# Kernel optimization log

Measured on AMD Instinct MI355X. Metric: run time of the kernel, lower is better.

Reference implementation:

```python
import jax, jax.numpy as jnp
import numpy as np

C, NH, NP = 512, 8, 4
HD = C // NH
H = W = D = 20
N = H * W * D
B = 2
EPS = 1e-5


def _layer_norm(x, g, b):
    mu = jnp.mean(x, axis=-1, keepdims=True)
    var = jnp.var(x, axis=-1, keepdims=True)
    return (x - mu) * jax.lax.rsqrt(var + EPS) * g + b


def setup_inputs() -> dict:
    key = jax.random.key(0)
    ks = jax.random.split(key, 10)

    def lin(k, fan_in, shape, scale=1.0):
        return (jax.random.normal(k, shape, jnp.float32) / np.float32(np.sqrt(fan_in))) * scale

    return {
        "f_query": jax.random.normal(ks[0], (B, C, H, W, D), jnp.float32),
        "f_kv": jax.random.normal(ks[1], (B, C, H, W, D), jnp.float32),
        "ln_g": jnp.ones((C,), jnp.float32),
        "ln_b": jnp.zeros((C,), jnp.float32),
        "Wq": lin(ks[2], C, (C, C)),
        "bq": jnp.zeros((C,), jnp.float32),
        "Wo1": lin(ks[3], C, (C, C)),
        "bo1": jnp.zeros((C,), jnp.float32),
        "Wo2": lin(ks[4], C, (C, NH * NP * 3), 0.1),  # small nonzero so interpolation is exercised
        "bo2": jnp.zeros((NH * NP * 3,), jnp.float32),
        "Wa": lin(ks[5], C, (C, NH * NP)),
        "ba": jnp.zeros((NH * NP,), jnp.float32),
        "Wout": lin(ks[6], C, (C, C)),
        "bout": jnp.zeros((C,), jnp.float32),
    }


def reference(f_query, f_kv, ln_g, ln_b, Wq, bq, Wo1, bo1, Wo2, bo2, Wa, ba, Wout, bout):
    # tokens: flatten (H,W,D) in row-major order, matching torch .flatten(2)
    fq = jnp.transpose(f_query.reshape(B, C, N), (0, 2, 1))  # (B,N,C)
    q = _layer_norm(fq, ln_g, ln_b)
    Q = q @ Wq + bq  # (B,N,C)

    off = jnp.clip(jax.nn.relu(Q @ Wo1 + bo1) @ Wo2 + bo2, -3.0, 3.0)
    off = off.reshape(B, N, NH, NP, 3)
    attn = jax.nn.softmax((Q @ Wa + ba).reshape(B, N, NH, NP), axis=-1)

    gy, gx, gz = jnp.meshgrid(jnp.arange(H, dtype=jnp.float32),
                              jnp.arange(W, dtype=jnp.float32),
                              jnp.arange(D, dtype=jnp.float32), indexing='ij')
    base = jnp.stack([gy, gx, gz], -1).reshape(N, 3)  # (N,3) in (y,x,z)
    locs = base[None, :, None, None, :] + off         # (B,N,NH,NP,3)

    # normalization exactly as original module (ch0 by H, ch1 by W, ch2 by D)
    n0 = 2.0 * locs[..., 0] / (H - 1) - 1.0
    n1 = 2.0 * locs[..., 1] / (W - 1) - 1.0
    n2 = 2.0 * locs[..., 2] / (D - 1) - 1.0
    # torch grid_sample on input permuted to (B,c,D,H,W): grid ch0->x (W axis),
    # ch1->y (H axis), ch2->z (D axis); align_corners=True; border padding = clip
    ix = jnp.clip((n0 + 1.0) * 0.5 * (W - 1), 0.0, W - 1)
    iy = jnp.clip((n1 + 1.0) * 0.5 * (H - 1), 0.0, H - 1)
    iz = jnp.clip((n2 + 1.0) * 0.5 * (D - 1), 0.0, D - 1)

    x0 = jnp.floor(ix); y0 = jnp.floor(iy); z0 = jnp.floor(iz)
    fx = (ix - x0)[..., None]; fy = (iy - y0)[..., None]; fz = (iz - z0)[..., None]
    x0i = x0.astype(jnp.int32); y0i = y0.astype(jnp.int32); z0i = z0.astype(jnp.int32)
    x1i = jnp.minimum(x0i + 1, W - 1)
    y1i = jnp.minimum(y0i + 1, H - 1)
    z1i = jnp.minimum(z0i + 1, D - 1)

    # f_kv (B,C,H,W,D) -> per-head channels-last volume (B,NH,D,H,W,HD)
    feats = jnp.transpose(f_kv.reshape(B, NH, HD, H, W, D), (0, 1, 5, 3, 4, 2))
    bi = jnp.arange(B)[:, None, None, None]
    hi = jnp.arange(NH)[None, None, :, None]

    def g(zi, yi, xi):
        return feats[bi, hi, zi, yi, xi]  # (B,N,NH,NP,HD)

    sampled = (
        g(z0i, y0i, x0i) * (1 - fz) * (1 - fy) * (1 - fx)
        + g(z0i, y0i, x1i) * (1 - fz) * (1 - fy) * fx
        + g(z0i, y1i, x0i) * (1 - fz) * fy * (1 - fx)
        + g(z0i, y1i, x1i) * (1 - fz) * fy * fx
        + g(z1i, y0i, x0i) * fz * (1 - fy) * (1 - fx)
        + g(z1i, y0i, x1i) * fz * (1 - fy) * fx
        + g(z1i, y1i, x0i) * fz * fy * (1 - fx)
        + g(z1i, y1i, x1i) * fz * fy * fx
    )  # (B,N,NH,NP,HD)

    out = jnp.einsum('bnhp,bnhpc->bnhc', attn, sampled).reshape(B, N, C)
    out = out @ Wout + bout
    return jnp.transpose(out, (0, 2, 1)).reshape(B, C, H, W, D)
```

## Files before the change

### kernel.cpp

```cpp
#include <hip/hip_runtime.h>
#include <math.h>

#define C_DIM 512
#define NHEAD 8
#define HDIM 64
#define NTOK 8000
#define BN_TOK 16000

typedef __attribute__((ext_vector_type(8))) _Float16 f16x8;
typedef __attribute__((ext_vector_type(4))) float f32x4;
typedef __attribute__((ext_vector_type(2))) _Float16 h2;
typedef unsigned short u16;

__device__ __forceinline__ int imin(int a, int b) { return a < b ? a : b; }

__device__ __forceinline__ u16 f2h(float x) {
    _Float16 h = (_Float16)x;
    return __builtin_bit_cast(u16, h);
}

__device__ __forceinline__ size_t aidx(int t, int c) {
    return ((size_t)(t >> 4)) * 8192 + (size_t)((c >> 5) * 512
         + (((c >> 3) & 3) * 128) + ((t & 15) * 8) + (c & 7));
}
__device__ __forceinline__ size_t bidx(int n, int k) {
    return ((size_t)(n >> 4)) * 8192 + (size_t)((k >> 5) * 512
         + (((k >> 3) & 3) * 128) + ((n & 15) * 8) + (k & 7));
}

__device__ __forceinline__ void async16(const void* g, void* l) {
    __builtin_amdgcn_global_load_lds(
        (const __attribute__((address_space(1))) void*)g,
        (__attribute__((address_space(3))) void*)l, 16, 0, 0);
}

__device__ __forceinline__ f32x4 agload16(const u16* p) {
    f32x4 r;
    asm volatile("global_load_dwordx4 %0, %1, off" : "=v"(r) : "v"(p));
    return r;
}

#define VMWAIT(N) do { asm volatile("s_waitcnt vmcnt(" #N ")"); \
                       __builtin_amdgcn_sched_barrier(0); } while (0)

__global__ __launch_bounds__(256) void transpose_c2l_f16(
    const float* __restrict__ in, u16* __restrict__ out)
{
    __shared__ float tile[32][33];
    int b = blockIdx.z;
    const float* inb = in + (size_t)b * 512 * NTOK;
    u16* outb = out + (size_t)b * NTOK * 512;
    int s0 = blockIdx.x * 32, r0 = blockIdx.y * 32;
    int tx = threadIdx.x & 31, ty = threadIdx.x >> 5;
#pragma unroll
    for (int i = 0; i < 4; i++)
        tile[ty + i * 8][tx] = inb[(size_t)(r0 + ty + i * 8) * NTOK + s0 + tx];
    __syncthreads();
    int rq = threadIdx.x & 7, sy = threadIdx.x >> 3;
    ushort4 o;
    o.x = f2h(tile[rq * 4 + 0][sy]);
    o.y = f2h(tile[rq * 4 + 1][sy]);
    o.z = f2h(tile[rq * 4 + 2][sy]);
    o.w = f2h(tile[rq * 4 + 3][sy]);
    *reinterpret_cast<ushort4*>(outb + (size_t)(s0 + sy) * 512 + r0 + rq * 4) = o;
}

__global__ __launch_bounds__(256) void wcvt_all(
    const float* __restrict__ W0, u16* __restrict__ T0,
    const float* __restrict__ W1, u16* __restrict__ T1,
    const float* __restrict__ W2, u16* __restrict__ T2,
    const float* __restrict__ W3, u16* __restrict__ T3,
    const float* __restrict__ W4, u16* __restrict__ T4)
{
    const float* W; u16* Wt; int Nout, Npad;
    switch (blockIdx.z) {
        case 0: W = W0; Wt = T0; Nout = 512; Npad = 512; break;
        case 1: W = W1; Wt = T1; Nout = 512; Npad = 512; break;
        case 2: W = W2; Wt = T2; Nout = 512; Npad = 512; break;
        case 3: W = W3; Wt = T3; Nout = 96;  Npad = 128; break;
        default: W = W4; Wt = T4; Nout = 32; Npad = 128; break;
    }
    int blocked = (blockIdx.z != 2);
    int n0 = blockIdx.x * 32, k0 = blockIdx.y * 32;
    if (n0 >= Npad) return;
    __shared__ float t[32][33];
    int tx = threadIdx.x & 31, ty = threadIdx.x >> 5;
#pragma unroll
    for (int i = 0; i < 4; i++) {
        int k = k0 + ty + i * 8, n = n0 + tx;
        t[ty + i * 8][tx] = (n < Nout) ? W[(size_t)k * Nout + n] : 0.f;
    }
    __syncthreads();
#pragma unroll
    for (int i = 0; i < 4; i++) {
        int n = n0 + ty + i * 8, k = k0 + tx;
        u16 v = f2h(t[tx][ty + i * 8]);
        if (blocked) Wt[bidx(n, k)] = v;
        else         Wt[(size_t)n * 512 + k] = v;
    }
}

__device__ __forceinline__ void lds_gemm64(
    const u16* Tin, u16* Tout, const u16* __restrict__ Wblk,
    const float* __restrict__ bias, int relu, int lane, int wv)
{
    int ml = lane & 15, quad = lane >> 4;
    int c0 = wv * 64;
    const u16* Bp = Wblk + (size_t)(c0 >> 4) * 8192 + (size_t)lane * 8;

    f32x4 acc[4][4];
#pragma unroll
    for (int t = 0; t < 4; t++)
#pragma unroll
        for (int j = 0; j < 4; j++) acc[t][j] = (f32x4){0.f, 0.f, 0.f, 0.f};

    f32x4 bfr[4][4];
#pragma unroll
    for (int kb = 0; kb < 3; kb++)
#pragma unroll
        for (int j = 0; j < 4; j++)
            bfr[kb][j] = agload16(Bp + (size_t)j * 8192 + kb * 512);

#pragma unroll
    for (int kk = 0; kk < 16; kk++) {
        if (kk + 3 < 16) {
#pragma unroll
            for (int j = 0; j < 4; j++)
                bfr[(kk + 3) & 3][j] = agload16(
                    Bp + (size_t)j * 8192 + (kk + 3) * 512);
        }
        f16x8 a[4];
#pragma unroll
        for (int t = 0; t < 4; t++)
            a[t] = *reinterpret_cast<const f16x8*>(
                Tin + (t * 16 + ml) * 520 + (kk * 4 + quad) * 8);
        if (kk < 13)       VMWAIT(12);
        else if (kk == 13) VMWAIT(8);
        else if (kk == 14) VMWAIT(4);
        else               VMWAIT(0);
#pragma unroll
        for (int j = 0; j < 4; j++) {
            f16x8 bj = __builtin_bit_cast(f16x8, bfr[kk & 3][j]);
#pragma unroll
            for (int t = 0; t < 4; t++)
                acc[t][j] = __builtin_amdgcn_mfma_f32_16x16x32_f16(
                    a[t], bj, acc[t][j], 0, 0, 0);
        }
    }

#pragma unroll
    for (int t = 0; t < 4; t++)
#pragma unroll
        for (int j = 0; j < 4; j++) {
            int col = c0 + j * 16 + ml;
            float bia = bias[col];
#pragma unroll
            for (int rg = 0; rg < 4; rg++) {
                float v = acc[t][j][rg] + bia;
                if (relu) v = fmaxf(v, 0.f);
                Tout[(t * 16 + quad * 4 + rg) * 520 + col] = f2h(v);
            }
        }
}

__global__ __launch_bounds__(512, 2) void mlp_fused(
    const float* __restrict__ fq, const float* __restrict__ gamma,
    const float* __restrict__ beta,
    const u16* __restrict__ Wqb, const float* __restrict__ bq,
    const u16* __restrict__ Wo1b, const float* __restrict__ bo1,
    const u16* __restrict__ Wo2b, const float* __restrict__ bo2,
    const u16* __restrict__ Wab, const float* __restrict__ ba,
    float* __restrict__ offb, float* __restrict__ lgb)
{
    __shared__ u16 T0[64 * 520], T1[64 * 520];
    __shared__ float ps[64][9], pq[64][9];
    __shared__ float muA[64], rsA[64];
    int tid = threadIdx.x, lane = tid & 63, wv = tid >> 6;
    int blk = blockIdx.x;
    int tp = tid & 63;
    int cg = tid >> 6;
    int b = blk >= 125;
    int n0 = (blk - b * 125) * 64;
    const float* src = fq + (size_t)b * C_DIM * NTOK + n0 + tp;

    float vals[64];
    {
        float s = 0.f, q = 0.f;
#pragma unroll
        for (int it = 0; it < 8; ++it) {
            int c0 = (cg + it * 8) * 8;
#pragma unroll
            for (int e = 0; e < 8; ++e) {
                float v = src[(size_t)(c0 + e) * NTOK];
                vals[it * 8 + e] = v;
                s += v; q += v * v;
            }
        }
        ps[tp][cg] = s; pq[tp][cg] = q;
    }
    __syncthreads();
    if (tid < 64) {
        float S = 0.f, SQ = 0.f;
#pragma unroll
        for (int g = 0; g < 8; ++g) { S += ps[tid][g]; SQ += pq[tid][g]; }
        float mu = S * (1.f / 512.f);
        muA[tid] = mu;
        rsA[tid] = rsqrtf(SQ * (1.f / 512.f) - mu * mu + 1e-5f);
    }
    __syncthreads();
    {
        float mu = muA[tp], rs = rsA[tp];
#pragma unroll
        for (int it = 0; it < 8; ++it) {
            int c0 = (cg + it * 8) * 8;
            u16 o[8];
#pragma unroll
            for (int e = 0; e < 8; ++e)
                o[e] = f2h((vals[it * 8 + e] - mu) * rs * gamma[c0 + e]
                           + beta[c0 + e]);
            *reinterpret_cast<f16x8*>(&T0[tp * 520 + c0]) =
                *reinterpret_cast<const f16x8*>(o);
        }
    }
    __syncthreads();
    lds_gemm64(T0, T1, Wqb, bq, 0, lane, wv);
    __syncthreads();
    lds_gemm64(T1, T0, Wo1b, bo1, 1, lane, wv);
    __syncthreads();
    {
        int ml = lane & 15, quad = lane >> 4;
        int isLg = wv >= 6;
        int cb = isLg ? (wv - 6) : wv;
        const u16* Tin = isLg ? T1 : T0;
        const u16* Wsm = isLg ? Wab : Wo2b;
        const float* bs = isLg ? ba : bo2;
        float* outg = isLg ? lgb : offb;
        int ldo = isLg ? 32 : 96;
        const u16* Wp = Wsm + (size_t)cb * 8192 + (size_t)lane * 8;
        f16x8 wb[16];
#pragma unroll
        for (int kk = 0; kk < 16; kk++)
            wb[kk] = *reinterpret_cast<const f16x8*>(Wp + (size_t)kk * 512);
        float bia = bs[cb * 16 + ml];
        int tbase = blk * 64;
#pragma unroll
        for (int tg = 0; tg < 4; tg++) {
            f32x4 acc = (f32x4){0.f, 0.f, 0.f, 0.f};
            const u16* Ar = Tin + (tg * 16 + ml) * 520;
#pragma unroll
            for (int kk = 0; kk < 16; kk++) {
                f16x8 af = *reinterpret_cast<const f16x8*>(
                    Ar + (kk * 4 + quad) * 8);
                acc = __builtin_amdgcn_mfma_f32_16x16x32_f16(
                    af, wb[kk], acc, 0, 0, 0);
            }
#pragma unroll
            for (int rg = 0; rg < 4; rg++)
                outg[(size_t)(tbase + tg * 16 + quad * 4 + rg) * ldo
                     + cb * 16 + ml] = acc[rg] + bia;
        }
    }
}

__device__ __forceinline__ void ws_body512(
    const u16* __restrict__ A, const u16* __restrict__ Bp,
    const float* __restrict__ bias, float* __restrict__ Cf,
    int colBase, int mt)
{
    __shared__ u16 Bs[64 * 512];
    int tid = threadIdx.x, lane = tid & 63, wv = tid >> 6;

#pragma unroll
    for (int c = 0; c < 8; c++) {
        int id = c * 512 + tid;
        int row = id >> 6, seg = id & 63;
        async16(Bp + (size_t)row * 512 + ((seg ^ (row & 7)) << 3),
                Bs + (size_t)id * 8);
    }

    int ml = lane & 15, quad = lane >> 4;
    int wm = (wv >> 1) * 64, wn = (wv & 1) * 32;

    int rowj[2];
#pragma unroll
    for (int j = 0; j < 2; j++) rowj[j] = wn + j * 16 + ml;

    __syncthreads();

    int bm = mt * 256;
    const u16* Ap = A + ((size_t)((bm + wm) >> 4)) * 8192 + (size_t)lane * 8;

    f32x4 acc[4][2];
#pragma unroll
    for (int i = 0; i < 4; i++)
#pragma unroll
        for (int j = 0; j < 2; j++) acc[i][j] = (f32x4){0.f, 0.f, 0.f, 0.f};

    f32x4 afr[4][4];
    f16x8 bf[2][2];

#pragma unroll
    for (int kb = 0; kb < 3; kb++)
#pragma unroll
        for (int i = 0; i < 4; i++)
            afr[kb][i] = agload16(Ap + (size_t)i * 8192 + kb * 512);
#pragma unroll
    for (int j = 0; j < 2; j++)
        bf[0][j] = *reinterpret_cast<const f16x8*>(
            Bs + (size_t)rowj[j] * 512 + (((0 + quad) ^ (rowj[j] & 7)) << 3));

#pragma unroll
    for (int kk = 0; kk < 16; kk++) {
        if (kk + 3 < 16) {
#pragma unroll
            for (int i = 0; i < 4; i++)
                afr[(kk + 3) & 3][i] = agload16(
                    Ap + (size_t)i * 8192 + (kk + 3) * 512);
        }
        if (kk + 1 < 16) {
#pragma unroll
            for (int j = 0; j < 2; j++) {
                int seg = (kk + 1) * 4 + quad;
                bf[(kk + 1) & 1][j] = *reinterpret_cast<const f16x8*>(
                    Bs + (size_t)rowj[j] * 512 + ((seg ^ (rowj[j] & 7)) << 3));
            }
        }
        if (kk < 13)       VMWAIT(12);
        else if (kk == 13) VMWAIT(8);
        else if (kk == 14) VMWAIT(4);
        else               VMWAIT(0);
#pragma unroll
        for (int i = 0; i < 4; i++)
#pragma unroll
            for (int j = 0; j < 2; j++)
                acc[i][j] = __builtin_amdgcn_mfma_f32_16x16x32_f16(
                    __builtin_bit_cast(f16x8, afr[kk & 3][i]),
                    bf[kk & 1][j], acc[i][j], 0, 0, 0);
    }

#pragma unroll
    for (int i = 0; i < 4; i++) {
        int row = bm + wm + i * 16 + quad * 4;
        if (row >= BN_TOK) continue;
#pragma unroll
        for (int j = 0; j < 2; j++) {
            int col = colBase + wn + j * 16 + ml;
            float bia = bias[col];
            int bb = row >= 8000;
            float4 st;
            st.x = acc[i][j][0] + bia;
            st.y = acc[i][j][1] + bia;
            st.z = acc[i][j][2] + bia;
            st.w = acc[i][j][3] + bia;
            *reinterpret_cast<float4*>(
                Cf + ((size_t)(bb * 512 + col)) * 8000 + (row - bb * 8000)) = st;
        }
    }
}

__global__ __launch_bounds__(512, 4) void gemm_out(
    const u16* __restrict__ A, const u16* __restrict__ WT,
    const float* __restrict__ bias, float* __restrict__ Cf)
{
    int did = blockIdx.x;
    int m = ((did >> 6) << 3) | (did & 7);
    if (m >= 63) return;
    int p = (did >> 3) & 7;
    ws_body512(A, WT + (size_t)p * 64 * 512, bias, Cf, p * 64, m);
}

__global__ __launch_bounds__(256) void sample_kernel(
    const u16* __restrict__ vol, const float* __restrict__ offb,
    const float* __restrict__ lgb, u16* __restrict__ outp)
{
    int wid = threadIdx.x >> 6, lane = threadIdx.x & 63;
    int bx = blockIdx.x;
    int bn = ((bx & 7) * 500 + (bx >> 3)) * 4 + wid;
    int h = lane >> 3, cl = lane & 7;
    int b = bn / NTOK, n = bn - b * NTOK;
    int y = n / 400;
    int r2 = n - y * 400;
    int x = r2 / 20;
    int z = r2 - x * 20;

    const float* op = offb + (size_t)bn * 96 + h * 12;
    const float* lp = lgb + (size_t)bn * 32 + h * 4;
    float l0 = lp[0], l1 = lp[1], l2 = lp[2], l3 = lp[3];
    float mx = fmaxf(fmaxf(l0, l1), fmaxf(l2, l3));
    float e0 = expf(l0 - mx), e1 = expf(l1 - mx), e2 = expf(l2 - mx), e3 = expf(l3 - mx);
    float inv = 1.f / (e0 + e1 + e2 + e3);
    float at[4] = {e0 * inv, e1 * inv, e2 * inv, e3 * inv};

    const u16* volb = vol + b * (NTOK * C_DIM) + h * HDIM + cl * 8;
    h2 acc0 = (h2)(_Float16)0, acc1 = acc0, acc2 = acc0, acc3 = acc0;
#pragma unroll 1
    for (int p = 0; p < 4; p++) {
        float o0 = fminf(fmaxf(op[p * 3 + 0], -3.f), 3.f);
        float o1 = fminf(fmaxf(op[p * 3 + 1], -3.f), 3.f);
        float o2 = fminf(fmaxf(op[p * 3 + 2], -3.f), 3.f);
        float ix = fminf(fmaxf((float)y + o0, 0.f), 19.f);
        float iy = fminf(fmaxf((float)x + o1, 0.f), 19.f);
        float iz = fminf(fmaxf((float)z + o2, 0.f), 19.f);
        float xf = floorf(ix), yf = floorf(iy), zf = floorf(iz);
        float fx = ix - xf, fy = iy - yf, fz = iz - zf;
        int x0 = (int)xf, y0 = (int)yf, z0 = (int)zf;
        int x1 = imin(x0 + 1, 19), y1 = imin(y0 + 1, 19), z1 = imin(z0 + 1, 19);
        int s00 = y0 * 400 + x0 * 20, s01 = y0 * 400 + x1 * 20;
        int s10 = y1 * 400 + x0 * 20, s11 = y1 * 400 + x1 * 20;
        uint4 v000 = *(const uint4*)(volb + (s00 + z0) * C_DIM);
        uint4 v001 = *(const uint4*)(volb + (s01 + z0) * C_DIM);
        uint4 v010 = *(const uint4*)(volb + (s10 + z0) * C_DIM);
        uint4 v011 = *(const uint4*)(volb + (s11 + z0) * C_DIM);
        uint4 v100 = *(const uint4*)(volb + (s00 + z1) * C_DIM);
        uint4 v101 = *(const uint4*)(volb + (s01 + z1) * C_DIM);
        uint4 v110 = *(const uint4*)(volb + (s10 + z1) * C_DIM);
        uint4 v111 = *(const uint4*)(volb + (s11 + z1) * C_DIM);
        float wz0 = (1.f - fz) * at[p], wz1 = fz * at[p];
        float w00 = wz0 * (1.f - fy), w01 = wz0 * fy;
        float w10 = wz1 * (1.f - fy), w11 = wz1 * fy;
        float gx0 = 1.f - fx;
        float cw[8] = { w00 * gx0, w00 * fx, w01 * gx0, w01 * fx,
                        w10 * gx0, w10 * fx, w11 * gx0, w11 * fx };
        const uint4* cv[8] = { &v000, &v001, &v010, &v011,
                               &v100, &v101, &v110, &v111 };
#pragma unroll
        for (int c = 0; c < 8; c++) {
            _Float16 wh = (_Float16)cw[c];
            h2 w2; w2.x = wh; w2.y = wh;
            uint4 d = *cv[c];
            acc0 += __builtin_bit_cast(h2, d.x) * w2;
            acc1 += __builtin_bit_cast(h2, d.y) * w2;
            acc2 += __builtin_bit_cast(h2, d.z) * w2;
            acc3 += __builtin_bit_cast(h2, d.w) * w2;
        }
    }
    uint4 o;
    o.x = __builtin_bit_cast(unsigned, acc0);
    o.y = __builtin_bit_cast(unsigned, acc1);
    o.z = __builtin_bit_cast(unsigned, acc2);
    o.w = __builtin_bit_cast(unsigned, acc3);
    *reinterpret_cast<uint4*>(outp + aidx(bn, h * HDIM + cl * 8)) = o;
}

extern "C" void kernel_launch(void* const* d_in, const int* in_sizes, int n_in,
                              void* d_out, int out_size, void* d_ws, size_t ws_size,
                              hipStream_t stream)
{
    const float* f_query = (const float*)d_in[0];
    const float* f_kv    = (const float*)d_in[1];
    const float* ln_g    = (const float*)d_in[2];
    const float* ln_b    = (const float*)d_in[3];
    const float* Wq      = (const float*)d_in[4];
    const float* bq      = (const float*)d_in[5];
    const float* Wo1     = (const float*)d_in[6];
    const float* bo1     = (const float*)d_in[7];
    const float* Wo2     = (const float*)d_in[8];
    const float* bo2     = (const float*)d_in[9];
    const float* Wa      = (const float*)d_in[10];
    const float* ba      = (const float*)d_in[11];
    const float* Wout    = (const float*)d_in[12];
    const float* bout    = (const float*)d_in[13];
    float* out = (float*)d_out;

    float* ws = (float*)d_ws;
    float* offb = ws;
    float* lgb  = ws + 1536000;
    u16* kvT   = (u16*)(ws + 2048000);
    u16* qb    = kvT  + 8192000;
    u16* WqT   = qb   + 8192000;
    u16* Wo1T  = WqT + 262144;
    u16* WoutT = Wo1T + 262144;
    u16* Wo2T  = WoutT + 262144;
    u16* WaT   = Wo2T + 65536;

    dim3 blk(256);
    dim3 blk512(512);
    wcvt_all<<<dim3(16, 16, 5), blk, 0, stream>>>(
        Wq, WqT, Wo1, Wo1T, Wout, WoutT, Wo2, Wo2T, Wa, WaT);
    transpose_c2l_f16<<<dim3(250, 16, 2), blk, 0, stream>>>(f_kv, kvT);
    mlp_fused<<<dim3(250), blk512, 0, stream>>>(
        f_query, ln_g, ln_b, WqT, bq, Wo1T, bo1, Wo2T, bo2, WaT, ba,
        offb, lgb);
    sample_kernel<<<dim3(4000), blk, 0, stream>>>(kvT, offb, lgb, qb);
    gemm_out<<<dim3(512), blk512, 0, stream>>>(qb, WoutT, bout, out);
}
```

Measured before the change: 194.8 us.

## Fuse trilinear sampling with output projection and merge prep kernels

The deformable sampling now writes each 64-token tile into LDS and immediately multiplies it by Wout with MFMA in the same block, so the separate sampled-feature buffer and the gemm_out kernel go away. The weight conversion and the f_kv transpose are merged into one launch. This removes a 16 MB intermediate write and read plus two kernel launches. In exchange only 250 blocks of 512 threads do the gather-heavy sampling, where the old sampling kernel used 4000 blocks, so latency hiding and occupancy during the gather may suffer. The Wout layout also changes from row-major to blocked.

```diff
diff --git a/kernel.cpp b/kernel.cpp
--- a/kernel.cpp
+++ b/kernel.cpp
@@ -19,19 +19,9 @@
     return __builtin_bit_cast(u16, h);
 }
 
-__device__ __forceinline__ size_t aidx(int t, int c) {
-    return ((size_t)(t >> 4)) * 8192 + (size_t)((c >> 5) * 512
-         + (((c >> 3) & 3) * 128) + ((t & 15) * 8) + (c & 7));
-}
 __device__ __forceinline__ size_t bidx(int n, int k) {
     return ((size_t)(n >> 4)) * 8192 + (size_t)((k >> 5) * 512
          + (((k >> 3) & 3) * 128) + ((n & 15) * 8) + (k & 7));
-}
-
-__device__ __forceinline__ void async16(const void* g, void* l) {
-    __builtin_amdgcn_global_load_lds(
-        (const __attribute__((address_space(1))) void*)g,
-        (__attribute__((address_space(3))) void*)l, 16, 0, 0);
 }
 
 __device__ __forceinline__ f32x4 agload16(const u16* p) {
@@ -43,60 +33,60 @@
 #define VMWAIT(N) do { asm volatile("s_waitcnt vmcnt(" #N ")"); \
                        __builtin_amdgcn_sched_barrier(0); } while (0)
 
-__global__ __launch_bounds__(256) void transpose_c2l_f16(
-    const float* __restrict__ in, u16* __restrict__ out)
+__global__ __launch_bounds__(256) void prep_all(
+    const float* __restrict__ f_kv, u16* __restrict__ kvT,
+    const float* __restrict__ W0, u16* __restrict__ T0w,
+    const float* __restrict__ W1, u16* __restrict__ T1w,
+    const float* __restrict__ W2, u16* __restrict__ T2w,
+    const float* __restrict__ W3, u16* __restrict__ T3w,
+    const float* __restrict__ W4, u16* __restrict__ T4w)
 {
     __shared__ float tile[32][33];
-    int b = blockIdx.z;
-    const float* inb = in + (size_t)b * 512 * NTOK;
-    u16* outb = out + (size_t)b * NTOK * 512;
-    int s0 = blockIdx.x * 32, r0 = blockIdx.y * 32;
-    int tx = threadIdx.x & 31, ty = threadIdx.x >> 5;
-#pragma unroll
-    for (int i = 0; i < 4; i++)
-        tile[ty + i * 8][tx] = inb[(size_t)(r0 + ty + i * 8) * NTOK + s0 + tx];
-    __syncthreads();
-    int rq = threadIdx.x & 7, sy = threadIdx.x >> 3;
-    ushort4 o;
-    o.x = f2h(tile[rq * 4 + 0][sy]);
-    o.y = f2h(tile[rq * 4 + 1][sy]);
-    o.z = f2h(tile[rq * 4 + 2][sy]);
-    o.w = f2h(tile[rq * 4 + 3][sy]);
-    *reinterpret_cast<ushort4*>(outb + (size_t)(s0 + sy) * 512 + r0 + rq * 4) = o;
-}
-
-__global__ __launch_bounds__(256) void wcvt_all(
-    const float* __restrict__ W0, u16* __restrict__ T0,
-    const float* __restrict__ W1, u16* __restrict__ T1,
-    const float* __restrict__ W2, u16* __restrict__ T2,
-    const float* __restrict__ W3, u16* __restrict__ T3,
-    const float* __restrict__ W4, u16* __restrict__ T4)
-{
-    const float* W; u16* Wt; int Nout, Npad;
-    switch (blockIdx.z) {
-        case 0: W = W0; Wt = T0; Nout = 512; Npad = 512; break;
-        case 1: W = W1; Wt = T1; Nout = 512; Npad = 512; break;
-        case 2: W = W2; Wt = T2; Nout = 512; Npad = 512; break;
-        case 3: W = W3; Wt = T3; Nout = 96;  Npad = 128; break;
-        default: W = W4; Wt = T4; Nout = 32; Npad = 128; break;
-    }
-    int blocked = (blockIdx.z != 2);
-    int n0 = blockIdx.x * 32, k0 = blockIdx.y * 32;
-    if (n0 >= Npad) return;
-    __shared__ float t[32][33];
-    int tx = threadIdx.x & 31, ty = threadIdx.x >> 5;
-#pragma unroll
-    for (int i = 0; i < 4; i++) {
-        int k = k0 + ty + i * 8, n = n0 + tx;
-        t[ty + i * 8][tx] = (n < Nout) ? W[(size_t)k * Nout + n] : 0.f;
-    }
-    __syncthreads();
-#pragma unroll
-    for (int i = 0; i < 4; i++) {
-        int n = n0 + ty + i * 8, k = k0 + tx;
-        u16 v = f2h(t[tx][ty + i * 8]);
-        if (blocked) Wt[bidx(n, k)] = v;
-        else         Wt[(size_t)n * 512 + k] = v;
+    int id = blockIdx.x;
+    if (id < 8000) {
+        int b = id / 4000, r = id - b * 4000;
+        int s0 = (r % 250) * 32, r0 = (r / 250) * 32;
+        const float* inb = f_kv + (size_t)b * 512 * NTOK;
+        u16* outb = kvT + (size_t)b * NTOK * 512;
+        int tx = threadIdx.x & 31, ty = threadIdx.x >> 5;
+#pragma unroll
+        for (int i = 0; i < 4; i++)
+            tile[ty + i * 8][tx] =
+                inb[(size_t)(r0 + ty + i * 8) * NTOK + s0 + tx];
+        __syncthreads();
+        int rq = threadIdx.x & 7, sy = threadIdx.x >> 3;
+        ushort4 o;
+        o.x = f2h(tile[rq * 4 + 0][sy]);
+        o.y = f2h(tile[rq * 4 + 1][sy]);
+        o.z = f2h(tile[rq * 4 + 2][sy]);
+        o.w = f2h(tile[rq * 4 + 3][sy]);
+        *reinterpret_cast<ushort4*>(
+            outb + (size_t)(s0 + sy) * 512 + r0 + rq * 4) = o;
+    } else {
+        int id2 = id - 8000;
+        int z = id2 >> 8, xy = id2 & 255;
+        int n0 = (xy & 15) * 32, k0 = (xy >> 4) * 32;
+        const float* W; u16* Wt; int Nout, Npad;
+        switch (z) {
+            case 0: W = W0; Wt = T0w; Nout = 512; Npad = 512; break;
+            case 1: W = W1; Wt = T1w; Nout = 512; Npad = 512; break;
+            case 2: W = W2; Wt = T2w; Nout = 512; Npad = 512; break;
+            case 3: W = W3; Wt = T3w; Nout = 96;  Npad = 128; break;
+            default: W = W4; Wt = T4w; Nout = 32; Npad = 128; break;
+        }
+        if (n0 >= Npad) return;
+        int tx = threadIdx.x & 31, ty = threadIdx.x >> 5;
+#pragma unroll
+        for (int i = 0; i < 4; i++) {
+            int k = k0 + ty + i * 8, n = n0 + tx;
+            tile[ty + i * 8][tx] = (n < Nout) ? W[(size_t)k * Nout + n] : 0.f;
+        }
+        __syncthreads();
+#pragma unroll
+        for (int i = 0; i < 4; i++) {
+            int n = n0 + ty + i * 8, k = k0 + tx;
+            Wt[bidx(n, k)] = f2h(tile[tx][ty + i * 8]);
+        }
     }
 }
 
@@ -262,184 +252,155 @@
     }
 }
 
-__device__ __forceinline__ void ws_body512(
-    const u16* __restrict__ A, const u16* __restrict__ Bp,
-    const float* __restrict__ bias, float* __restrict__ Cf,
-    int colBase, int mt)
+__global__ __launch_bounds__(512, 2) void sample_out(
+    const u16* __restrict__ vol, const float* __restrict__ offb,
+    const float* __restrict__ lgb, const u16* __restrict__ Woutb,
+    const float* __restrict__ bout, float* __restrict__ outp)
 {
-    __shared__ u16 Bs[64 * 512];
+    __shared__ u16 T0[64 * 520];
     int tid = threadIdx.x, lane = tid & 63, wv = tid >> 6;
-
-#pragma unroll
-    for (int c = 0; c < 8; c++) {
-        int id = c * 512 + tid;
-        int row = id >> 6, seg = id & 63;
-        async16(Bp + (size_t)row * 512 + ((seg ^ (row & 7)) << 3),
-                Bs + (size_t)id * 8);
-    }
-
-    int ml = lane & 15, quad = lane >> 4;
-    int wm = (wv >> 1) * 64, wn = (wv & 1) * 32;
-
-    int rowj[2];
-#pragma unroll
-    for (int j = 0; j < 2; j++) rowj[j] = wn + j * 16 + ml;
-
-    __syncthreads();
-
-    int bm = mt * 256;
-    const u16* Ap = A + ((size_t)((bm + wm) >> 4)) * 8192 + (size_t)lane * 8;
-
-    f32x4 acc[4][2];
-#pragma unroll
-    for (int i = 0; i < 4; i++)
-#pragma unroll
-        for (int j = 0; j < 2; j++) acc[i][j] = (f32x4){0.f, 0.f, 0.f, 0.f};
-
-    f32x4 afr[4][4];
-    f16x8 bf[2][2];
-
-#pragma unroll
-    for (int kb = 0; kb < 3; kb++)
-#pragma unroll
-        for (int i = 0; i < 4; i++)
-            afr[kb][i] = agload16(Ap + (size_t)i * 8192 + kb * 512);
-#pragma unroll
-    for (int j = 0; j < 2; j++)
-        bf[0][j] = *reinterpret_cast<const f16x8*>(
-            Bs + (size_t)rowj[j] * 512 + (((0 + quad) ^ (rowj[j] & 7)) << 3));
-
-#pragma unroll
-    for (int kk = 0; kk < 16; kk++) {
-        if (kk + 3 < 16) {
-#pragma unroll
-            for (int i = 0; i < 4; i++)
-                afr[(kk + 3) & 3][i] = agload16(
-                    Ap + (size_t)i * 8192 + (kk + 3) * 512);
-        }
-        if (kk + 1 < 16) {
-#pragma unroll
-            for (int j = 0; j < 2; j++) {
-                int seg = (kk + 1) * 4 + quad;
-                bf[(kk + 1) & 1][j] = *reinterpret_cast<const f16x8*>(
-                    Bs + (size_t)rowj[j] * 512 + ((seg ^ (rowj[j] & 7)) << 3));
-            }
-        }
-        if (kk < 13)       VMWAIT(12);
-        else if (kk == 13) VMWAIT(8);
-        else if (kk == 14) VMWAIT(4);
-        else               VMWAIT(0);
-#pragma unroll
-        for (int i = 0; i < 4; i++)
-#pragma unroll
-            for (int j = 0; j < 2; j++)
-                acc[i][j] = __builtin_amdgcn_mfma_f32_16x16x32_f16(
-                    __builtin_bit_cast(f16x8, afr[kk & 3][i]),
-                    bf[kk & 1][j], acc[i][j], 0, 0, 0);
-    }
-
-#pragma unroll
-    for (int i = 0; i < 4; i++) {
-        int row = bm + wm + i * 16 + quad * 4;
-        if (row >= BN_TOK) continue;
-#pragma unroll
-        for (int j = 0; j < 2; j++) {
-            int col = colBase + wn + j * 16 + ml;
-            float bia = bias[col];
-            int bb = row >= 8000;
-            float4 st;
-            st.x = acc[i][j][0] + bia;
-            st.y = acc[i][j][1] + bia;
-            st.z = acc[i][j][2] + bia;
-            st.w = acc[i][j][3] + bia;
-            *reinterpret_cast<float4*>(
-                Cf + ((size_t)(bb * 512 + col)) * 8000 + (row - bb * 8000)) = st;
-        }
-    }
-}
-
-__global__ __launch_bounds__(512, 4) void gemm_out(
-    const u16* __restrict__ A, const u16* __restrict__ WT,
-    const float* __restrict__ bias, float* __restrict__ Cf)
-{
-    int did = blockIdx.x;
-    int m = ((did >> 6) << 3) | (did & 7);
-    if (m >= 63) return;
-    int p = (did >> 3) & 7;
-    ws_body512(A, WT + (size_t)p * 64 * 512, bias, Cf, p * 64, m);
-}
-
-__global__ __launch_bounds__(256) void sample_kernel(
-    const u16* __restrict__ vol, const float* __restrict__ offb,
-    const float* __restrict__ lgb, u16* __restrict__ outp)
-{
-    int wid = threadIdx.x >> 6, lane = threadIdx.x & 63;
-    int bx = blockIdx.x;
-    int bn = ((bx & 7) * 500 + (bx >> 3)) * 4 + wid;
-    int h = lane >> 3, cl = lane & 7;
-    int b = bn / NTOK, n = bn - b * NTOK;
-    int y = n / 400;
-    int r2 = n - y * 400;
-    int x = r2 / 20;
-    int z = r2 - x * 20;
-
-    const float* op = offb + (size_t)bn * 96 + h * 12;
-    const float* lp = lgb + (size_t)bn * 32 + h * 4;
-    float l0 = lp[0], l1 = lp[1], l2 = lp[2], l3 = lp[3];
-    float mx = fmaxf(fmaxf(l0, l1), fmaxf(l2, l3));
-    float e0 = expf(l0 - mx), e1 = expf(l1 - mx), e2 = expf(l2 - mx), e3 = expf(l3 - mx);
-    float inv = 1.f / (e0 + e1 + e2 + e3);
-    float at[4] = {e0 * inv, e1 * inv, e2 * inv, e3 * inv};
-
-    const u16* volb = vol + b * (NTOK * C_DIM) + h * HDIM + cl * 8;
-    h2 acc0 = (h2)(_Float16)0, acc1 = acc0, acc2 = acc0, acc3 = acc0;
+    int orig = blockIdx.x;
+    int xcd = orig & 7, slot = orig >> 3;
+    int w = (xcd < 2 ? xcd * 32 : 64 + (xcd - 2) * 31) + slot;
+    int tbase = w * 64;
+
+    {
+        int h = lane >> 3, cl = lane & 7;
 #pragma unroll 1
-    for (int p = 0; p < 4; p++) {
-        float o0 = fminf(fmaxf(op[p * 3 + 0], -3.f), 3.f);
-        float o1 = fminf(fmaxf(op[p * 3 + 1], -3.f), 3.f);
-        float o2 = fminf(fmaxf(op[p * 3 + 2], -3.f), 3.f);
-        float ix = fminf(fmaxf((float)y + o0, 0.f), 19.f);
-        float iy = fminf(fmaxf((float)x + o1, 0.f), 19.f);
-        float iz = fminf(fmaxf((float)z + o2, 0.f), 19.f);
-        float xf = floorf(ix), yf = floorf(iy), zf = floorf(iz);
-        float fx = ix - xf, fy = iy - yf, fz = iz - zf;
-        int x0 = (int)xf, y0 = (int)yf, z0 = (int)zf;
-        int x1 = imin(x0 + 1, 19), y1 = imin(y0 + 1, 19), z1 = imin(z0 + 1, 19);
-        int s00 = y0 * 400 + x0 * 20, s01 = y0 * 400 + x1 * 20;
-        int s10 = y1 * 400 + x0 * 20, s11 = y1 * 400 + x1 * 20;
-        uint4 v000 = *(const uint4*)(volb + (s00 + z0) * C_DIM);
-        uint4 v001 = *(const uint4*)(volb + (s01 + z0) * C_DIM);
-        uint4 v010 = *(const uint4*)(volb + (s10 + z0) * C_DIM);
-        uint4 v011 = *(const uint4*)(volb + (s11 + z0) * C_DIM);
-        uint4 v100 = *(const uint4*)(volb + (s00 + z1) * C_DIM);
-        uint4 v101 = *(const uint4*)(volb + (s01 + z1) * C_DIM);
-        uint4 v110 = *(const uint4*)(volb + (s10 + z1) * C_DIM);
-        uint4 v111 = *(const uint4*)(volb + (s11 + z1) * C_DIM);
-        float wz0 = (1.f - fz) * at[p], wz1 = fz * at[p];
-        float w00 = wz0 * (1.f - fy), w01 = wz0 * fy;
-        float w10 = wz1 * (1.f - fy), w11 = wz1 * fy;
-        float gx0 = 1.f - fx;
-        float cw[8] = { w00 * gx0, w00 * fx, w01 * gx0, w01 * fx,
-                        w10 * gx0, w10 * fx, w11 * gx0, w11 * fx };
-        const uint4* cv[8] = { &v000, &v001, &v010, &v011,
-                               &v100, &v101, &v110, &v111 };
-#pragma unroll
-        for (int c = 0; c < 8; c++) {
-            _Float16 wh = (_Float16)cw[c];
-            h2 w2; w2.x = wh; w2.y = wh;
-            uint4 d = *cv[c];
-            acc0 += __builtin_bit_cast(h2, d.x) * w2;
-            acc1 += __builtin_bit_cast(h2, d.y) * w2;
-            acc2 += __builtin_bit_cast(h2, d.z) * w2;
-            acc3 += __builtin_bit_cast(h2, d.w) * w2;
-        }
-    }
-    uint4 o;
-    o.x = __builtin_bit_cast(unsigned, acc0);
-    o.y = __builtin_bit_cast(unsigned, acc1);
-    o.z = __builtin_bit_cast(unsigned, acc2);
-    o.w = __builtin_bit_cast(unsigned, acc3);
-    *reinterpret_cast<uint4*>(outp + aidx(bn, h * HDIM + cl * 8)) = o;
+        for (int tt = 0; tt < 8; ++tt) {
+            int trow = wv * 8 + tt;
+            int bn = tbase + trow;
+            int b = bn >= NTOK;
+            int n = bn - b * NTOK;
+            int y = n / 400;
+            int r2 = n - y * 400;
+            int x = r2 / 20;
+            int z = r2 - x * 20;
+            const float* op = offb + (size_t)bn * 96 + h * 12;
+            const float* lp = lgb + (size_t)bn * 32 + h * 4;
+            float l0 = lp[0], l1 = lp[1], l2 = lp[2], l3 = lp[3];
+            float mx = fmaxf(fmaxf(l0, l1), fmaxf(l2, l3));
+            float e0 = expf(l0 - mx), e1 = expf(l1 - mx);
+            float e2 = expf(l2 - mx), e3 = expf(l3 - mx);
+            float inv = 1.f / (e0 + e1 + e2 + e3);
+            float at[4] = {e0 * inv, e1 * inv, e2 * inv, e3 * inv};
+            const u16* volb = vol + b * (NTOK * C_DIM) + h * HDIM + cl * 8;
+            h2 acc0 = (h2)(_Float16)0, acc1 = acc0, acc2 = acc0, acc3 = acc0;
+#pragma unroll
+            for (int p = 0; p < 4; p++) {
+                float o0 = fminf(fmaxf(op[p * 3 + 0], -3.f), 3.f);
+                float o1 = fminf(fmaxf(op[p * 3 + 1], -3.f), 3.f);
+                float o2 = fminf(fmaxf(op[p * 3 + 2], -3.f), 3.f);
+                float ix = fminf(fmaxf((float)y + o0, 0.f), 19.f);
+                float iy = fminf(fmaxf((float)x + o1, 0.f), 19.f);
+                float iz = fminf(fmaxf((float)z + o2, 0.f), 19.f);
+                float xf = floorf(ix), yf = floorf(iy), zf = floorf(iz);
+                float fx = ix - xf, fy = iy - yf, fz = iz - zf;
+                int x0 = (int)xf, y0 = (int)yf, z0 = (int)zf;
+                int x1 = imin(x0 + 1, 19), y1 = imin(y0 + 1, 19);
+                int z1 = imin(z0 + 1, 19);
+                int s00 = y0 * 400 + x0 * 20, s01 = y0 * 400 + x1 * 20;
+                int s10 = y1 * 400 + x0 * 20, s11 = y1 * 400 + x1 * 20;
+                uint4 v000 = *(const uint4*)(volb + (s00 + z0) * C_DIM);
+                uint4 v001 = *(const uint4*)(volb + (s01 + z0) * C_DIM);
+                uint4 v010 = *(const uint4*)(volb + (s10 + z0) * C_DIM);
+                uint4 v011 = *(const uint4*)(volb + (s11 + z0) * C_DIM);
+                uint4 v100 = *(const uint4*)(volb + (s00 + z1) * C_DIM);
+                uint4 v101 = *(const uint4*)(volb + (s01 + z1) * C_DIM);
+                uint4 v110 = *(const uint4*)(volb + (s10 + z1) * C_DIM);
+                uint4 v111 = *(const uint4*)(volb + (s11 + z1) * C_DIM);
+                float wz0 = (1.f - fz) * at[p], wz1 = fz * at[p];
+                float w00 = wz0 * (1.f - fy), w01 = wz0 * fy;
+                float w10 = wz1 * (1.f - fy), w11 = wz1 * fy;
+                float gx0 = 1.f - fx;
+                float cw[8] = { w00 * gx0, w00 * fx, w01 * gx0, w01 * fx,
+                                w10 * gx0, w10 * fx, w11 * gx0, w11 * fx };
+                const uint4* cv[8] = { &v000, &v001, &v010, &v011,
+                                       &v100, &v101, &v110, &v111 };
+#pragma unroll
+                for (int c = 0; c < 8; c++) {
+                    _Float16 wh = (_Float16)cw[c];
+                    h2 w2; w2.x = wh; w2.y = wh;
+                    uint4 d = *cv[c];
+                    acc0 += __builtin_bit_cast(h2, d.x) * w2;
+                    acc1 += __builtin_bit_cast(h2, d.y) * w2;
+                    acc2 += __builtin_bit_cast(h2, d.z) * w2;
+                    acc3 += __builtin_bit_cast(h2, d.w) * w2;
+                }
+            }
+            uint4 o;
+            o.x = __builtin_bit_cast(unsigned, acc0);
+            o.y = __builtin_bit_cast(unsigned, acc1);
+            o.z = __builtin_bit_cast(unsigned, acc2);
+            o.w = __builtin_bit_cast(unsigned, acc3);
+            *reinterpret_cast<uint4*>(&T0[trow * 520 + h * HDIM + cl * 8]) = o;
+        }
+    }
+    __syncthreads();
+
+    {
+        int ml = lane & 15, quad = lane >> 4;
+        int c0 = wv * 64;
+        const u16* Bp = Woutb + (size_t)(c0 >> 4) * 8192 + (size_t)lane * 8;
+
+        f32x4 acc[4][4];
+#pragma unroll
+        for (int t = 0; t < 4; t++)
+#pragma unroll
+            for (int j = 0; j < 4; j++) acc[t][j] = (f32x4){0.f, 0.f, 0.f, 0.f};
+
+        f32x4 bfr[4][4];
+#pragma unroll
+        for (int kb = 0; kb < 3; kb++)
+#pragma unroll
+            for (int j = 0; j < 4; j++)
+                bfr[kb][j] = agload16(Bp + (size_t)j * 8192 + kb * 512);
+
+#pragma unroll
+        for (int kk = 0; kk < 16; kk++) {
+            if (kk + 3 < 16) {
+#pragma unroll
+                for (int j = 0; j < 4; j++)
+                    bfr[(kk + 3) & 3][j] = agload16(
+                        Bp + (size_t)j * 8192 + (kk + 3) * 512);
+            }
+            f16x8 a[4];
+#pragma unroll
+            for (int t = 0; t < 4; t++)
+                a[t] = *reinterpret_cast<const f16x8*>(
+                    T0 + (t * 16 + ml) * 520 + (kk * 4 + quad) * 8);
+            if (kk < 13)       VMWAIT(12);
+            else if (kk == 13) VMWAIT(8);
+            else if (kk == 14) VMWAIT(4);
+            else               VMWAIT(0);
+#pragma unroll
+            for (int j = 0; j < 4; j++) {
+                f16x8 bj = __builtin_bit_cast(f16x8, bfr[kk & 3][j]);
+#pragma unroll
+                for (int t = 0; t < 4; t++)
+                    acc[t][j] = __builtin_amdgcn_mfma_f32_16x16x32_f16(
+                        a[t], bj, acc[t][j], 0, 0, 0);
+            }
+        }
+
+        int bb = tbase >= NTOK;
+        int tloc = tbase - bb * NTOK;
+#pragma unroll
+        for (int t = 0; t < 4; t++)
+#pragma unroll
+            for (int j = 0; j < 4; j++) {
+                int col = c0 + j * 16 + ml;
+                float bia = bout[col];
+                float4 st;
+                st.x = acc[t][j][0] + bia;
+                st.y = acc[t][j][1] + bia;
+                st.z = acc[t][j][2] + bia;
+                st.w = acc[t][j][3] + bia;
+                *reinterpret_cast<float4*>(
+                    outp + ((size_t)(bb * 512 + col)) * 8000
+                         + tloc + t * 16 + quad * 4) = st;
+            }
+    }
 }
 
 extern "C" void kernel_launch(void* const* d_in, const int* in_sizes, int n_in,
@@ -466,8 +427,7 @@
     float* offb = ws;
     float* lgb  = ws + 1536000;
     u16* kvT   = (u16*)(ws + 2048000);
-    u16* qb    = kvT  + 8192000;
-    u16* WqT   = qb   + 8192000;
+    u16* WqT   = kvT + 16384000;
     u16* Wo1T  = WqT + 262144;
     u16* WoutT = Wo1T + 262144;
     u16* Wo2T  = WoutT + 262144;
@@ -475,12 +435,11 @@
 
     dim3 blk(256);
     dim3 blk512(512);
-    wcvt_all<<<dim3(16, 16, 5), blk, 0, stream>>>(
-        Wq, WqT, Wo1, Wo1T, Wout, WoutT, Wo2, Wo2T, Wa, WaT);
-    transpose_c2l_f16<<<dim3(250, 16, 2), blk, 0, stream>>>(f_kv, kvT);
+    prep_all<<<dim3(9280), blk, 0, stream>>>(
+        f_kv, kvT, Wq, WqT, Wo1, Wo1T, Wout, WoutT, Wo2, Wo2T, Wa, WaT);
     mlp_fused<<<dim3(250), blk512, 0, stream>>>(
         f_query, ln_g, ln_b, WqT, bq, Wo1T, bo1, Wo2T, bo2, WaT, ba,
         offb, lgb);
-    sample_kernel<<<dim3(4000), blk, 0, stream>>>(kvT, offb, lgb, qb);
-    gemm_out<<<dim3(512), blk512, 0, stream>>>(qb, WoutT, bout, out);
-}
+    sample_out<<<dim3(250), blk512, 0, stream>>>(
+        kvT, offb, lgb, WoutT, bout, out);
+}
```

Result: faster. 179.6 us (-7.8%).
